# Kernel optimization log

Measured on AMD Instinct MI355X. Metric: run time of the kernel, lower is better.

The kernel has to match this reference:

```python
import jax, jax.numpy as jnp
import numpy as np


def ste_sign(x):
    # Forward: q(x) = +1 if x >= 0 else -1.
    # Backward: clipped straight-through estimator (identity on |x| <= 1).
    clipped = jnp.clip(x, -1.0, 1.0)
    binary = jnp.where(x >= 0, 1.0, -1.0).astype(x.dtype)
    return clipped + jax.lax.stop_gradient(binary - clipped)


BATCH = 16384
IN_FEATURES = 4096
UNITS = 512


def setup_inputs() -> dict:
    key = jax.random.key(0)
    kx, kw = jax.random.split(key)
    x = jax.random.normal(kx, (BATCH, IN_FEATURES), dtype=jnp.float32)
    # Latent full-precision kernel (kept in [-1,1]-ish range like a constrained BNN kernel)
    W = jax.random.normal(kw, (IN_FEATURES, UNITS), dtype=jnp.float32) * 0.5
    b = jnp.zeros((UNITS,), dtype=jnp.float32)
    return {"x": x, "W": W, "b": b}


def reference(x, W, b):
    # QuantizedDense: binarize inputs and kernel to +/-1, then standard dense matmul.
    xq = ste_sign(x)                # [B, F]
    Wq = ste_sign(W)                # [F, U]
    return jnp.dot(xq, Wq) + b      # [B, U]
```

## Files before the change

kernel.cpp:

```cpp
#include <hip/hip_runtime.h>
#include <stdint.h>


#define BATCH  16384
#define UNITS  512
#define KDIM   4096
#define KSTEP  64
#define NSTEP  (KDIM / KSTEP)
#define NPER   (NSTEP / 4)
#define MROWS  32

typedef int v4i  __attribute__((ext_vector_type(4)));
typedef int v16i __attribute__((ext_vector_type(16)));

__global__ __launch_bounds__(256) void pack_w_kernel(const float* __restrict__ W,
                                                     uint8_t* __restrict__ Wb2) {
    int t  = blockIdx.x * 256 + threadIdx.x;
    int n  = t & 511;
    int k0 = (t >> 9) * 8;
    unsigned long long m = 0;
    #pragma unroll
    for (int j = 0; j < 8; ++j) {
        float v = W[(size_t)(k0 + j) * UNITS + n];
        m |= ((v < 0.f) ? 0xFFull : 0x01ull) << (8 * j);
    }
    int s  = k0 >> 6;
    int kk = k0 & 63;
    int ks = kk >> 5;
    int hi = (kk & 31) >> 4;
    int lane = (n & 31) + 32 * hi;
    size_t a = ((((size_t)s * 16 + (n >> 5)) * 2 + ks) * 64 + lane) * 16 + (kk & 15);
    *reinterpret_cast<unsigned long long*>(Wb2 + a) = m;
}

__device__ __forceinline__ uint32_t sgn4(float4 v) {
    uint32_t b0 = v.x < 0.f ? 0xFFu : 0x01u;
    uint32_t b1 = v.y < 0.f ? 0xFFu : 0x01u;
    uint32_t b2 = v.z < 0.f ? 0xFFu : 0x01u;
    uint32_t b3 = v.w < 0.f ? 0xFFu : 0x01u;
    return b0 | (b1 << 8) | (b2 << 16) | (b3 << 24);
}

#define LOADB(D0, D1, D2, D3, S)                                               \
    {                                                                          \
        const uint8_t* _b = bbase + (size_t)(S) * 32768;                       \
        D0 = *reinterpret_cast<const v4i*>(_b);                                \
        D1 = *reinterpret_cast<const v4i*>(_b + 1024);                         \
        D2 = *reinterpret_cast<const v4i*>(_b + 2048);                         \
        D3 = *reinterpret_cast<const v4i*>(_b + 3072);                         \
    }

#define CLUSTER(PB, FI0, FI1, B0, B1, B2, B3)                                  \
    {                                                                          \
        v4i af0 = *reinterpret_cast<const v4i*>(&Af[(PB) * 8192 + (FI0) * 1024 + l * 16]); \
        v4i af1 = *reinterpret_cast<const v4i*>(&Af[(PB) * 8192 + (FI1) * 1024 + l * 16]); \
        __builtin_amdgcn_s_setprio(1);                                         \
        acc0 = __builtin_amdgcn_mfma_i32_32x32x32_i8(af0, B0, acc0, 0, 0, 0);  \
        acc0 = __builtin_amdgcn_mfma_i32_32x32x32_i8(af1, B1, acc0, 0, 0, 0);  \
        acc1 = __builtin_amdgcn_mfma_i32_32x32x32_i8(af0, B2, acc1, 0, 0, 0);  \
        acc1 = __builtin_amdgcn_mfma_i32_32x32x32_i8(af1, B3, acc1, 0, 0, 0);  \
        __builtin_amdgcn_s_setprio(0);                                         \
    }

#define PERIOD(Q, PB)                                                          \
    {                                                                          \
        const int _s4 = 4 * (Q) + 4;                                           \
        LOADB(bp1a, bp1b, bp1c, bp1d, 4 * (Q) + 1);                            \
        CLUSTER(PB, 0, 1, bp0a, bp0b, bp0c, bp0d);                             \
        float4 xq0 = *reinterpret_cast<const float4*>(                         \
            xrow + (size_t)((_s4     < NSTEP) ? _s4     : NSTEP - 1) * KSTEP); \
        float4 xq1 = *reinterpret_cast<const float4*>(                         \
            xrow + (size_t)((_s4 + 1 < NSTEP) ? _s4 + 1 : NSTEP - 1) * KSTEP); \
        LOADB(bp0a, bp0b, bp0c, bp0d, 4 * (Q) + 2);                            \
        CLUSTER(PB, 2, 3, bp1a, bp1b, bp1c, bp1d);                             \
        float4 xq2 = *reinterpret_cast<const float4*>(                         \
            xrow + (size_t)((_s4 + 2 < NSTEP) ? _s4 + 2 : NSTEP - 1) * KSTEP); \
        float4 xq3 = *reinterpret_cast<const float4*>(                         \
            xrow + (size_t)((_s4 + 3 < NSTEP) ? _s4 + 3 : NSTEP - 1) * KSTEP); \
        LOADB(bp1a, bp1b, bp1c, bp1d, 4 * (Q) + 3);                            \
        CLUSTER(PB, 4, 5, bp0a, bp0b, bp0c, bp0d);                             \
        LOADB(bp0a, bp0b, bp0c, bp0d, (_s4 < NSTEP) ? _s4 : NSTEP - 1);        \
        CLUSTER(PB, 6, 7, bp1a, bp1b, bp1c, bp1d);                             \
        uint8_t* _aw = afw + ((PB) ^ 1) * 8192;                                \
        *reinterpret_cast<uint32_t*>(_aw)        = sgn4(xq0);                  \
        *reinterpret_cast<uint32_t*>(_aw + 2048) = sgn4(xq1);                  \
        *reinterpret_cast<uint32_t*>(_aw + 4096) = sgn4(xq2);                  \
        *reinterpret_cast<uint32_t*>(_aw + 6144) = sgn4(xq3);                  \
        __syncthreads();                                                       \
    }

__global__ __launch_bounds__(512, 1) void mm_kernel(const float* __restrict__ x,
                                                    const uint8_t* __restrict__ Wb2,
                                                    const float* __restrict__ bias,
                                                    float* __restrict__ C) {
    __shared__ __attribute__((aligned(16))) uint8_t Af[2 * 8 * 1024];
    const int t   = threadIdx.x;
    const int l   = t & 63;
    const int wv  = t >> 6;
    const int lr  = l & 31;
    const int hi  = l >> 5;
    const int row0 = blockIdx.x * MROWS;
    const int ar = t >> 4;
    const int ak = (t & 15) * 4;
    const int a_lane = (ar & 31) + 32 * ((ak >> 4) & 1);
    const int a_ks   = ak >> 5;
    const int a_off  = ak & 15;
    uint8_t* afw = &Af[a_ks * 1024 + a_lane * 16 + a_off];
    const float* xrow = x + (size_t)(row0 + ar) * KDIM + ak;
    const uint8_t* bbase = Wb2 + ((size_t)(wv * 2) * 2 * 64 + l) * 16;

    v16i acc0, acc1;
    #pragma unroll
    for (int e = 0; e < 16; ++e) { acc0[e] = 0; acc1[e] = 0; }

    v4i bp0a, bp0b, bp0c, bp0d, bp1a, bp1b, bp1c, bp1d;

    {
        LOADB(bp0a, bp0b, bp0c, bp0d, 0);
        float4 x0 = *reinterpret_cast<const float4*>(xrow);
        float4 x1 = *reinterpret_cast<const float4*>(xrow + KSTEP);
        float4 x2 = *reinterpret_cast<const float4*>(xrow + 2 * KSTEP);
        float4 x3 = *reinterpret_cast<const float4*>(xrow + 3 * KSTEP);
        *reinterpret_cast<uint32_t*>(afw)        = sgn4(x0);
        *reinterpret_cast<uint32_t*>(afw + 2048) = sgn4(x1);
        *reinterpret_cast<uint32_t*>(afw + 4096) = sgn4(x2);
        *reinterpret_cast<uint32_t*>(afw + 6144) = sgn4(x3);
        __syncthreads();
    }

    #pragma unroll 1
    for (int q = 0; q < NPER; q += 2) {
        PERIOD(q,     0);
        PERIOD(q + 1, 1);
    }

    #pragma unroll
    for (int ct = 0; ct < 2; ++ct) {
        const int col = wv * 64 + ct * 32 + lr;
        const float bv = bias[col];
        const v16i& a = ct ? acc1 : acc0;
        #pragma unroll
        for (int r = 0; r < 16; ++r) {
            int row = row0 + (r & 3) + 8 * (r >> 2) + 4 * hi;
            C[(size_t)row * UNITS + col] = (float)a[r] + bv;
        }
    }
}

extern "C" void kernel_launch(void* const* d_in, const int* in_sizes, int n_in,
                              void* d_out, int out_size, void* d_ws, size_t ws_size,
                              hipStream_t stream) {
    const float* x = (const float*)d_in[0];
    const float* W = (const float*)d_in[1];
    const float* b = (const float*)d_in[2];
    float* out = (float*)d_out;

    uint8_t* Wb2 = (uint8_t*)d_ws;

    pack_w_kernel<<<(512 * 512) / 256, 256, 0, stream>>>(W, Wb2);
    mm_kernel<<<BATCH / MROWS, 512, 0, stream>>>(x, Wb2, b, out);
}
```

Before: 95.25 us.

## Split work across 16 waves per block with one accumulator tile each

Doubles the block to 1024 threads so each of 16 waves owns a single 32x32 output tile instead of two, halving per-wave accumulator and B-fragment registers. Launch bounds become (1024,2) so more waves can be resident and hide latency. The x-load and sign-pack work is redistributed so each thread handles two K sub-slices per period. The cost is fewer MFMAs per wave between barriers, relatively more sync overhead per block, and A fragments read from LDS by twice as many waves.

```diff
diff --git a/kernel.cpp b/kernel.cpp
--- a/kernel.cpp
+++ b/kernel.cpp
@@ -41,58 +41,48 @@
     return b0 | (b1 << 8) | (b2 << 16) | (b3 << 24);
 }
 
-#define LOADB(D0, D1, D2, D3, S)                                               \
+#define LOADB2(D0, D1, S)                                                      \
     {                                                                          \
         const uint8_t* _b = bbase + (size_t)(S) * 32768;                       \
         D0 = *reinterpret_cast<const v4i*>(_b);                                \
         D1 = *reinterpret_cast<const v4i*>(_b + 1024);                         \
-        D2 = *reinterpret_cast<const v4i*>(_b + 2048);                         \
-        D3 = *reinterpret_cast<const v4i*>(_b + 3072);                         \
     }
 
-#define CLUSTER(PB, FI0, FI1, B0, B1, B2, B3)                                  \
+#define CLUSTER(PB, SIP, B0, B1)                                               \
     {                                                                          \
-        v4i af0 = *reinterpret_cast<const v4i*>(&Af[(PB) * 8192 + (FI0) * 1024 + l * 16]); \
-        v4i af1 = *reinterpret_cast<const v4i*>(&Af[(PB) * 8192 + (FI1) * 1024 + l * 16]); \
+        v4i af0 = *reinterpret_cast<const v4i*>(                               \
+            &Af[(PB) * 8192 + ((SIP) * 2) * 1024 + l * 16]);                   \
+        v4i af1 = *reinterpret_cast<const v4i*>(                               \
+            &Af[(PB) * 8192 + ((SIP) * 2 + 1) * 1024 + l * 16]);               \
         __builtin_amdgcn_s_setprio(1);                                         \
-        acc0 = __builtin_amdgcn_mfma_i32_32x32x32_i8(af0, B0, acc0, 0, 0, 0);  \
-        acc0 = __builtin_amdgcn_mfma_i32_32x32x32_i8(af1, B1, acc0, 0, 0, 0);  \
-        acc1 = __builtin_amdgcn_mfma_i32_32x32x32_i8(af0, B2, acc1, 0, 0, 0);  \
-        acc1 = __builtin_amdgcn_mfma_i32_32x32x32_i8(af1, B3, acc1, 0, 0, 0);  \
+        acc = __builtin_amdgcn_mfma_i32_32x32x32_i8(af0, B0, acc, 0, 0, 0);    \
+        acc = __builtin_amdgcn_mfma_i32_32x32x32_i8(af1, B1, acc, 0, 0, 0);    \
         __builtin_amdgcn_s_setprio(0);                                         \
     }
 
 #define PERIOD(Q, PB)                                                          \
     {                                                                          \
-        const int _s4 = 4 * (Q) + 4;                                           \
-        LOADB(bp1a, bp1b, bp1c, bp1d, 4 * (Q) + 1);                            \
-        CLUSTER(PB, 0, 1, bp0a, bp0b, bp0c, bp0d);                             \
-        float4 xq0 = *reinterpret_cast<const float4*>(                         \
-            xrow + (size_t)((_s4     < NSTEP) ? _s4     : NSTEP - 1) * KSTEP); \
-        float4 xq1 = *reinterpret_cast<const float4*>(                         \
-            xrow + (size_t)((_s4 + 1 < NSTEP) ? _s4 + 1 : NSTEP - 1) * KSTEP); \
-        LOADB(bp0a, bp0b, bp0c, bp0d, 4 * (Q) + 2);                            \
-        CLUSTER(PB, 2, 3, bp1a, bp1b, bp1c, bp1d);                             \
-        float4 xq2 = *reinterpret_cast<const float4*>(                         \
-            xrow + (size_t)((_s4 + 2 < NSTEP) ? _s4 + 2 : NSTEP - 1) * KSTEP); \
-        float4 xq3 = *reinterpret_cast<const float4*>(                         \
-            xrow + (size_t)((_s4 + 3 < NSTEP) ? _s4 + 3 : NSTEP - 1) * KSTEP); \
-        LOADB(bp1a, bp1b, bp1c, bp1d, 4 * (Q) + 3);                            \
-        CLUSTER(PB, 4, 5, bp0a, bp0b, bp0c, bp0d);                             \
-        LOADB(bp0a, bp0b, bp0c, bp0d, (_s4 < NSTEP) ? _s4 : NSTEP - 1);        \
-        CLUSTER(PB, 6, 7, bp1a, bp1b, bp1c, bp1d);                             \
-        uint8_t* _aw = afw + ((PB) ^ 1) * 8192;                                \
-        *reinterpret_cast<uint32_t*>(_aw)        = sgn4(xq0);                  \
-        *reinterpret_cast<uint32_t*>(_aw + 2048) = sgn4(xq1);                  \
-        *reinterpret_cast<uint32_t*>(_aw + 4096) = sgn4(xq2);                  \
-        *reinterpret_cast<uint32_t*>(_aw + 6144) = sgn4(xq3);                  \
+        LOADB2(bn0, bn1, 4 * (Q) + 1);                                         \
+        CLUSTER(PB, 0, bp0, bp1);                                              \
+        const int _sc0 = (4 * (Q) + 4 + sp0 < NSTEP) ? 4 * (Q) + 4 + sp0 : NSTEP - 1; \
+        float4 xq0 = *reinterpret_cast<const float4*>(xp0 + (size_t)_sc0 * KSTEP);    \
+        LOADB2(bp0, bp1, 4 * (Q) + 2);                                         \
+        CLUSTER(PB, 1, bn0, bn1);                                              \
+        const int _sc1 = (4 * (Q) + 4 + sp1 < NSTEP) ? 4 * (Q) + 4 + sp1 : NSTEP - 1; \
+        float4 xq1 = *reinterpret_cast<const float4*>(xp1 + (size_t)_sc1 * KSTEP);    \
+        LOADB2(bn0, bn1, 4 * (Q) + 3);                                         \
+        CLUSTER(PB, 2, bp0, bp1);                                              \
+        LOADB2(bp0, bp1, (4 * (Q) + 4 < NSTEP) ? 4 * (Q) + 4 : NSTEP - 1);     \
+        CLUSTER(PB, 3, bn0, bn1);                                              \
+        *reinterpret_cast<uint32_t*>(&Af[((PB) ^ 1) * 8192 + aw0]) = sgn4(xq0);\
+        *reinterpret_cast<uint32_t*>(&Af[((PB) ^ 1) * 8192 + aw1]) = sgn4(xq1);\
         __syncthreads();                                                       \
     }
 
-__global__ __launch_bounds__(512, 1) void mm_kernel(const float* __restrict__ x,
-                                                    const uint8_t* __restrict__ Wb2,
-                                                    const float* __restrict__ bias,
-                                                    float* __restrict__ C) {
+__global__ __launch_bounds__(1024, 2) void mm_kernel(const float* __restrict__ x,
+                                                     const uint8_t* __restrict__ Wb2,
+                                                     const float* __restrict__ bias,
+                                                     float* __restrict__ C) {
     __shared__ __attribute__((aligned(16))) uint8_t Af[2 * 8 * 1024];
     const int t   = threadIdx.x;
     const int l   = t & 63;
@@ -100,31 +90,31 @@
     const int lr  = l & 31;
     const int hi  = l >> 5;
     const int row0 = blockIdx.x * MROWS;
-    const int ar = t >> 4;
-    const int ak = (t & 15) * 4;
-    const int a_lane = (ar & 31) + 32 * ((ak >> 4) & 1);
-    const int a_ks   = ak >> 5;
-    const int a_off  = ak & 15;
-    uint8_t* afw = &Af[a_ks * 1024 + a_lane * 16 + a_off];
-    const float* xrow = x + (size_t)(row0 + ar) * KDIM + ak;
-    const uint8_t* bbase = Wb2 + ((size_t)(wv * 2) * 2 * 64 + l) * 16;
 
-    v16i acc0, acc1;
+    const int sp0 = t >> 9;
+    const int sp1 = (t + 1024) >> 9;
+    const int fa0 = t & 511;
+    const int ar0 = fa0 >> 4, ak0 = (fa0 & 15) * 4;
+    const int aw0 = (sp0 * 2 + (ak0 >> 5)) * 1024
+                  + ((ar0 & 31) + 32 * ((ak0 >> 4) & 1)) * 16 + (ak0 & 15);
+    const int aw1 = (sp1 * 2 + (ak0 >> 5)) * 1024
+                  + ((ar0 & 31) + 32 * ((ak0 >> 4) & 1)) * 16 + (ak0 & 15);
+    const float* xp0 = x + (size_t)(row0 + ar0) * KDIM + ak0;
+    const float* xp1 = xp0;
+    const uint8_t* bbase = Wb2 + wv * 2048 + (size_t)l * 16;
+
+    v16i acc;
     #pragma unroll
-    for (int e = 0; e < 16; ++e) { acc0[e] = 0; acc1[e] = 0; }
+    for (int e = 0; e < 16; ++e) acc[e] = 0;
 
-    v4i bp0a, bp0b, bp0c, bp0d, bp1a, bp1b, bp1c, bp1d;
+    v4i bp0, bp1, bn0, bn1;
 
     {
-        LOADB(bp0a, bp0b, bp0c, bp0d, 0);
-        float4 x0 = *reinterpret_cast<const float4*>(xrow);
-        float4 x1 = *reinterpret_cast<const float4*>(xrow + KSTEP);
-        float4 x2 = *reinterpret_cast<const float4*>(xrow + 2 * KSTEP);
-        float4 x3 = *reinterpret_cast<const float4*>(xrow + 3 * KSTEP);
-        *reinterpret_cast<uint32_t*>(afw)        = sgn4(x0);
-        *reinterpret_cast<uint32_t*>(afw + 2048) = sgn4(x1);
-        *reinterpret_cast<uint32_t*>(afw + 4096) = sgn4(x2);
-        *reinterpret_cast<uint32_t*>(afw + 6144) = sgn4(x3);
+        LOADB2(bp0, bp1, 0);
+        float4 xq0 = *reinterpret_cast<const float4*>(xp0 + (size_t)sp0 * KSTEP);
+        float4 xq1 = *reinterpret_cast<const float4*>(xp1 + (size_t)sp1 * KSTEP);
+        *reinterpret_cast<uint32_t*>(&Af[aw0]) = sgn4(xq0);
+        *reinterpret_cast<uint32_t*>(&Af[aw1]) = sgn4(xq1);
         __syncthreads();
     }
 
@@ -134,15 +124,13 @@
         PERIOD(q + 1, 1);
     }
 
-    #pragma unroll
-    for (int ct = 0; ct < 2; ++ct) {
-        const int col = wv * 64 + ct * 32 + lr;
+    {
+        const int col = wv * 32 + lr;
         const float bv = bias[col];
-        const v16i& a = ct ? acc1 : acc0;
         #pragma unroll
         for (int r = 0; r < 16; ++r) {
             int row = row0 + (r & 3) + 8 * (r >> 2) + 4 * hi;
-            C[(size_t)row * UNITS + col] = (float)a[r] + bv;
+            C[(size_t)row * UNITS + col] = (float)acc[r] + bv;
         }
     }
 }
@@ -158,5 +146,5 @@
     uint8_t* Wb2 = (uint8_t*)d_ws;
 
     pack_w_kernel<<<(512 * 512) / 256, 256, 0, stream>>>(W, Wb2);
-    mm_kernel<<<BATCH / MROWS, 512, 0, stream>>>(x, Wb2, b, out);
+    mm_kernel<<<BATCH / MROWS, 1024, 0, stream>>>(x, Wb2, b, out);
 }
```

After: 114.0 us. 19.7% more time.
